# Performance work log

Measured on AMD Instinct MI355X. Metric: run time of the kernel, lower is better.

## Reference

```python
import jax, jax.numpy as jnp
import numpy as np

B, S, D = 32, 512, 512
H, DK, DV, DFF = 8, 64, 64, 2048
TEMP = float(np.sqrt(DK))  # d_k ** 0.5
COS_EPS = 1e-8             # torch.cosine_similarity eps
LN_EPS = 1e-5


def _layernorm(x, g, b):
    mu = jnp.mean(x, axis=-1, keepdims=True)
    var = jnp.var(x, axis=-1, keepdims=True)
    return (x - mu) * jax.lax.rsqrt(var + LN_EPS) * g + b


def setup_inputs() -> dict:
    key = jax.random.key(0)
    ks = jax.random.split(key, 12)
    s = 0.02
    return {
        "x": jax.random.normal(ks[0], (B, S, D), dtype=jnp.float32),
        "w_q": jax.random.normal(ks[1], (D, H * DK), dtype=jnp.float32) * s,
        "w_k": jax.random.normal(ks[2], (D, H * DK), dtype=jnp.float32) * s,
        "w_v": jax.random.normal(ks[3], (D, H * DV), dtype=jnp.float32) * s,
        "w_o": jax.random.normal(ks[4], (H * DV, D), dtype=jnp.float32) * s,
        "w_ff1": jax.random.normal(ks[5], (D, DFF), dtype=jnp.float32) * s,
        "b_ff1": jnp.zeros((DFF,), dtype=jnp.float32),
        "w_ff2": jax.random.normal(ks[6], (DFF, D), dtype=jnp.float32) * s,
        "b_ff2": jnp.zeros((D,), dtype=jnp.float32),
        "g1": jnp.ones((D,), dtype=jnp.float32),
        "b1": jnp.zeros((D,), dtype=jnp.float32),
        "g2": jnp.ones((D,), dtype=jnp.float32),
        "b2": jnp.zeros((D,), dtype=jnp.float32),
    }


def reference(x, w_q, w_k, w_v, w_o, w_ff1, b_ff1, w_ff2, b_ff2, g1, b1, g2, b2):
    b, s, _ = x.shape
    # projections -> [b, h, s, d]
    q = (x @ w_q).reshape(b, s, H, DK).transpose(0, 2, 1, 3)
    k = (x @ w_k).reshape(b, s, H, DK).transpose(0, 2, 1, 3)
    v = (x @ w_v).reshape(b, s, H, DV).transpose(0, 2, 1, 3)
    # cosine-similarity attention: dot(q,k) / max(||q||*||k||, eps) / temperature
    scores = jnp.einsum("bhqd,bhkd->bhqk", q, k)
    nq = jnp.linalg.norm(q, axis=-1)  # [b,h,s]
    nk = jnp.linalg.norm(k, axis=-1)
    denom = jnp.maximum(nq[:, :, :, None] * nk[:, :, None, :], COS_EPS)
    attn = jax.nn.softmax(scores / denom / TEMP, axis=-1)
    out = jnp.einsum("bhqk,bhkd->bhqd", attn, v)  # [b,h,s,dv]
    out = out.transpose(0, 2, 1, 3).reshape(b, s, H * DV) @ w_o
    # residual + LN1
    h1 = _layernorm(x + out, g1, b1)
    # FFN
    ffn = jax.nn.relu(h1 @ w_ff1 + b_ff1) @ w_ff2 + b_ff2
    # residual + LN2
    return _layernorm(h1 + ffn, g2, b2)
```

## Files before the change

kernel.cpp:

```cpp
#include <hip/hip_runtime.h>
#include <cmath>

typedef __bf16 bf16x8 __attribute__((ext_vector_type(8)));
typedef __bf16 bf16x4 __attribute__((ext_vector_type(4)));
typedef float  floatx4 __attribute__((ext_vector_type(4)));

#define LN_EPS 1e-5f
#define INV_TEMP 0.125f

static const int Mrows = 16384;

__device__ __forceinline__ void gload_lds16(const void* g, void* l) {
  __builtin_amdgcn_global_load_lds(
      (const __attribute__((address_space(1))) void*)g,
      (__attribute__((address_space(3))) void*)l, 16, 0, 0);
}

__global__ __launch_bounds__(256) void prep_kernel(const float* __restrict__ x, __bf16* __restrict__ xb,
                                                   const float* __restrict__ wq, const float* __restrict__ wk,
                                                   const float* __restrict__ wv, const float* __restrict__ wo,
                                                   const float* __restrict__ wff1, const float* __restrict__ wff2,
                                                   __bf16* __restrict__ tq, __bf16* __restrict__ tk,
                                                   __bf16* __restrict__ tv, __bf16* __restrict__ to_,
                                                   __bf16* __restrict__ tff1, __bf16* __restrict__ tff2) {
  const int bid = blockIdx.x, tid = threadIdx.x;
  if (bid < 8192) {
    int i = bid * 256 + tid;
    float4 v = ((const float4*)x)[i];
    __bf16* d = xb + i * 4;
    d[0] = (__bf16)v.x; d[1] = (__bf16)v.y; d[2] = (__bf16)v.z; d[3] = (__bf16)v.w;
    return;
  }
  __shared__ __bf16 til[64][72];
  int t = bid - 8192;
  const float* src; __bf16* dst; int R, C, bx, by;
  if (t < 256) {
    int w = t >> 6, tt = t & 63;
    const float* srcs[4] = {wq, wk, wv, wo};
    __bf16* dsts[4] = {tq, tk, tv, to_};
    src = srcs[w]; dst = dsts[w]; R = 512; C = 512; bx = tt & 7; by = tt >> 3;
  } else if (t < 512) {
    int tt = t - 256;
    src = wff1; dst = tff1; R = 512; C = 2048; bx = tt & 31; by = tt >> 5;
  } else {
    int tt = t - 512;
    src = wff2; dst = tff2; R = 2048; C = 512; bx = tt & 7; by = tt >> 3;
  }
  const float* s = src + (size_t)(by * 64) * C + bx * 64;
  int r = tid >> 4, c4 = (tid & 15) * 4;
  for (int p = 0; p < 4; ++p) {
    int rr = r + p * 16;
    float4 v = *(const float4*)(s + (size_t)rr * C + c4);
    til[c4 + 0][rr] = (__bf16)v.x;
    til[c4 + 1][rr] = (__bf16)v.y;
    til[c4 + 2][rr] = (__bf16)v.z;
    til[c4 + 3][rr] = (__bf16)v.w;
  }
  __syncthreads();
  __bf16* d = dst + (size_t)(bx * 64) * R + by * 64;
  int orow = tid >> 3, oc8 = (tid & 7) * 8;
  for (int p = 0; p < 2; ++p) {
    int rr = orow + p * 32;
    *(bf16x8*)(d + (size_t)rr * R + oc8) = *(const bf16x8*)(&til[rr][oc8]);
  }
}

template <int EPI, int NBN, int NDIM, int KDIM, int NKS>
__global__ __launch_bounds__(512, 2) void gemm256(const __bf16* __restrict__ A,
                                                  const __bf16* __restrict__ Bt,
                                                  __bf16* __restrict__ Cv,
                                                  const float* __restrict__ bias,
                                                  float* __restrict__ norms,
                                                  __bf16* __restrict__ vtg) {
  __shared__ __align__(16) char smem[131072];
  const int tid = threadIdx.x;
  const int wave = tid >> 6, lane = tid & 63;
  const int l15 = lane & 15, quad = lane >> 4;
  const int wm = wave >> 2, wn = wave & 3;

  constexpr int NBM = Mrows / 256;
  constexpr int NBLK = NBM * NBN * NKS;
  constexpr int KS = KDIM / NKS;
  constexpr int NTH = KS / 32;

  int id = blockIdx.x;
  int t = (id & 7) * (NBLK >> 3) + (id >> 3);
  const int ks = t / (NBM * NBN);
  t -= ks * (NBM * NBN);
  const int nblk = t % NBN, mblk = t / NBN;
  const int m0 = mblk * 256, n0 = nblk * 256;
  const __bf16* Ab = A + (size_t)ks * KS;
  const __bf16* Bb = Bt + (size_t)ks * KS;
  __bf16* Cw = Cv + (size_t)ks * Mrows * NDIM;
  (void)bias;

  const int wq = wave & 3, isB = wave >> 2;
  const int l3 = lane >> 3, s_ = lane & 7;
  const int rowst = wq * 64 + l3 * 2 + (s_ >> 2);
  const int ksw = (s_ & 3) ^ (l3 & 3);
  const __bf16* sbase = (isB ? Bb + (size_t)(n0 + rowst) * KDIM
                             : Ab + (size_t)(m0 + rowst) * KDIM) + ksw * 8;
  const int ldob = isB * 16384 + wq * 4096 + lane * 16;

  const int lrt = (l15 >> 1) * 128 + (((l15 & 1) * 4 + (quad ^ ((l15 >> 1) & 3))) * 16);
  const int aoff = wm * 8192;
  const int boff = 16384 + wn * 4096;

  floatx4 zero = {0.f, 0.f, 0.f, 0.f};
  floatx4 acc[8][4];
#pragma unroll
  for (int i = 0; i < 8; ++i)
#pragma unroll
    for (int j = 0; j < 4; ++j) acc[i][j] = zero;

#define STAGEH(h)                                                            \
  {                                                                          \
    _Pragma("unroll") for (int j = 0; j < 4; ++j)                            \
        gload_lds16(sbase + (size_t)j * (16 * KDIM) + (h) * 32,              \
                    smem + ((h) & 3) * 32768 + ldob + j * 1024);             \
  }

#define PHASE(h, VM, DOSTAGE)                                                \
  {                                                                          \
    asm volatile("s_waitcnt vmcnt(" #VM ")" ::: "memory");                   \
    __builtin_amdgcn_s_barrier();                                            \
    const char* slotp = smem + ((h) & 3) * 32768;                            \
    bf16x8 aF[8], bF[4];                                                     \
    _Pragma("unroll") for (int i = 0; i < 8; ++i)                            \
      aF[i] = *(const bf16x8*)(slotp + aoff + i * 1024 + lrt);               \
    _Pragma("unroll") for (int j = 0; j < 4; ++j)                            \
      bF[j] = *(const bf16x8*)(slotp + boff + j * 1024 + lrt);               \
    if (DOSTAGE) STAGEH((h) + 3);                                            \
    asm volatile("s_waitcnt lgkmcnt(0)" ::: "memory");                       \
    __builtin_amdgcn_s_setprio(1);                                           \
    _Pragma("unroll") for (int i = 0; i < 8; ++i)                            \
      _Pragma("unroll") for (int j = 0; j < 4; ++j)                          \
        acc[i][j] = __builtin_amdgcn_mfma_f32_16x16x32_bf16(aF[i], bF[j],    \
                                                            acc[i][j], 0, 0, 0); \
    __builtin_amdgcn_s_setprio(0);                                           \
  }

  STAGEH(0); STAGEH(1); STAGEH(2);

  for (int h = 0; h <= NTH - 4; ++h) PHASE(h, 8, 1);
  PHASE(NTH - 3, 8, 0);
  PHASE(NTH - 2, 4, 0);
  PHASE(NTH - 1, 0, 0);

#undef STAGEH
#undef PHASE

  if (EPI == 4) {
    int head_global = (n0 + wn * 64) >> 6;
    int kind = head_global >> 3;
    if (kind < 2) {
      int h = head_global & 7;
#pragma unroll
      for (int ii = 0; ii < 8; ++ii)
#pragma unroll
        for (int r = 0; r < 4; ++r) {
          float sq = 0.f;
#pragma unroll
          for (int jj = 0; jj < 4; ++jj) {
            float v = acc[ii][jj][r];
            sq += v * v;
          }
          for (int m = 1; m < 16; m <<= 1) sq += __shfl_xor(sq, m, 64);
          if (l15 == 0) {
            int arow = m0 + wm * 128 + ii * 16 + quad * 4 + r;
            int bb = arow >> 9, ss = arow & 511;
            norms[kind * 131072 + ((bb << 3) + h) * 512 + ss] = rsqrtf(sq);
          }
        }
    } else {
      const int PADT = 136;
      __bf16* Ct = (__bf16*)smem;
      int bb = m0 >> 9, s0r = m0 & 511;
#pragma unroll
      for (int hh = 0; hh < 2; ++hh) {
        __builtin_amdgcn_s_barrier();
        if (wm == hh) {
#pragma unroll
          for (int ii = 0; ii < 8; ++ii)
#pragma unroll
            for (int jj = 0; jj < 4; ++jj) {
              bf16x4 pk;
#pragma unroll
              for (int r = 0; r < 4; ++r) pk[r] = (__bf16)acc[ii][jj][r];
              *(bf16x4*)(Ct + (wn * 64 + jj * 16 + l15) * PADT + ii * 16 + quad * 4) = pk;
            }
        }
        __builtin_amdgcn_s_barrier();
#pragma unroll
        for (int p = 0; p < 8; ++p) {
          int c = p * 32 + (tid >> 4);
          int s8 = (tid & 15) * 8;
          int h = ((n0 + c) >> 6) & 7, d = c & 63;
          *(bf16x8*)(vtg + ((size_t)(((bb << 3) + h) * 64 + d)) * 512 + s0r + hh * 128 + s8) =
              *(const bf16x8*)(Ct + c * PADT + s8);
        }
      }
      return;
    }
  }

  const int PADC = 264;
  __bf16* Cs = (__bf16*)smem;
  float bv[4];
  if (EPI == 2) {
#pragma unroll
    for (int j = 0; j < 4; ++j) bv[j] = bias[n0 + wn * 64 + j * 16 + l15];
  }
#pragma unroll
  for (int hh = 0; hh < 2; ++hh) {
    __builtin_amdgcn_s_barrier();
    if (wm == hh) {
#pragma unroll
      for (int i = 0; i < 8; ++i)
#pragma unroll
        for (int j = 0; j < 4; ++j)
#pragma unroll
          for (int r = 0; r < 4; ++r) {
            float v = acc[i][j][r];
            if (EPI == 2) {
              v += bv[j];
              v = v > 0.f ? v : 0.f;
            }
            Cs[(i * 16 + quad * 4 + r) * PADC + wn * 64 + j * 16 + l15] = (__bf16)v;
          }
    }
    __builtin_amdgcn_s_barrier();
#pragma unroll
    for (int p = 0; p < 8; ++p) {
      int rowl = p * 16 + (tid >> 5);
      int c8 = (tid & 31) * 8;
      *(bf16x8*)(Cw + (size_t)(m0 + hh * 128 + rowl) * NDIM + n0 + c8) =
          *(const bf16x8*)(Cs + rowl * PADC + c8);
    }
  }
}

__global__ __launch_bounds__(256) void attn_kernel(const __bf16* __restrict__ qkv,
                                                   const __bf16* __restrict__ vtg,
                                                   const float* __restrict__ norms,
                                                   __bf16* __restrict__ out) {
  __shared__ __align__(16) __bf16 Ks[64 * 64];
  __shared__ __align__(16) __bf16 Vs[64 * 64];
  __shared__ __align__(16) __bf16 P2[4][16 * 72];
  const int tid = threadIdx.x, wave = tid >> 6, lane = tid & 63;
  const int l15 = lane & 15, quad = lane >> 4;
  const int bh = blockIdx.x & 255;
  const int qq = blockIdx.x >> 8;
  const int b = bh >> 3, h = bh & 7;
  const int qbase = qq * 128 + wave * 32;
  const int rs = lane >> 3;
  const int swz_st = ((lane & 7) ^ rs) * 8;
  const int s7 = l15 & 7;

  const __bf16* Qb = qkv + (size_t)(b * 512) * 1536 + h * 64;
  const __bf16* Kb = Qb + 512;
  const __bf16* Vtb = vtg + (size_t)bh * 32768;
  const float* nkinv = norms + 131072 + bh * 512;
  const float* nqinv = norms + bh * 512;
  __bf16* Pw = P2[wave];

  bf16x8 aq[2][2];
  float cq[2];
  for (int ch = 0; ch < 2; ++ch) {
    int qrow = qbase + ch * 16;
    aq[ch][0] = *(const bf16x8*)(Qb + (size_t)(qrow + l15) * 1536 + quad * 8);
    aq[ch][1] = *(const bf16x8*)(Qb + (size_t)(qrow + l15) * 1536 + 32 + quad * 8);
    cq[ch] = nqinv[qrow + l15] * INV_TEMP;
  }

  floatx4 zero = {0.f, 0.f, 0.f, 0.f};
  floatx4 o[2][4];
  float lsum[2] = {0.f, 0.f};
  for (int ch = 0; ch < 2; ++ch)
    for (int jd = 0; jd < 4; ++jd) o[ch][jd] = zero;

  for (int kt = 0; kt < 8; ++kt) {
    int s0 = kt * 64;
    __syncthreads();
    for (int c = 0; c < 4; ++c) {
      int g = wave * 4 + c;
      const __bf16* src;
      __bf16* dst;
      if (g < 8) {
        int sk = g * 8 + rs;
        src = Kb + (size_t)(s0 + sk) * 1536 + swz_st;
        dst = Ks + g * 512;
      } else {
        int g2 = g - 8;
        int d = g2 * 8 + rs;
        src = Vtb + (size_t)d * 512 + s0 + swz_st;
        dst = Vs + g2 * 512;
      }
      gload_lds16(src, dst + lane * 8);
    }
    __syncthreads();

    for (int ch = 0; ch < 2; ++ch) {
      floatx4 z[4];
      for (int j = 0; j < 4; ++j) {
        int r64 = (j * 16 + l15) * 64;
        bf16x8 k0 = *(const bf16x8*)(Ks + r64 + ((quad ^ s7) * 8));
        bf16x8 k1 = *(const bf16x8*)(Ks + r64 + (((4 + quad) ^ s7) * 8));
        floatx4 zz = zero;
        zz = __builtin_amdgcn_mfma_f32_16x16x32_bf16(k0, aq[ch][0], zz, 0, 0, 0);
        zz = __builtin_amdgcn_mfma_f32_16x16x32_bf16(k1, aq[ch][1], zz, 0, 0, 0);
        z[j] = zz;
      }
      for (int j = 0; j < 4; ++j) {
        floatx4 nk4 = *(const floatx4*)(nkinv + s0 + j * 16 + quad * 4);
        bf16x4 pk;
        for (int r = 0; r < 4; ++r) {
          float p = __expf(z[j][r] * cq[ch] * nk4[r]);
          lsum[ch] += p;
          pk[r] = (__bf16)p;
        }
        *(bf16x4*)(Pw + l15 * 72 + j * 16 + quad * 4) = pk;
      }
      bf16x8 ap0 = *(const bf16x8*)(Pw + l15 * 72 + quad * 8);
      bf16x8 ap1 = *(const bf16x8*)(Pw + l15 * 72 + 32 + quad * 8);
      for (int jd = 0; jd < 4; ++jd) {
        int r64 = (jd * 16 + l15) * 64;
        bf16x8 v0 = *(const bf16x8*)(Vs + r64 + ((quad ^ s7) * 8));
        bf16x8 v1 = *(const bf16x8*)(Vs + r64 + (((4 + quad) ^ s7) * 8));
        o[ch][jd] = __builtin_amdgcn_mfma_f32_16x16x32_bf16(v0, ap0, o[ch][jd], 0, 0, 0);
        o[ch][jd] = __builtin_amdgcn_mfma_f32_16x16x32_bf16(v1, ap1, o[ch][jd], 0, 0, 0);
      }
    }
  }

  for (int ch = 0; ch < 2; ++ch) {
    float s = lsum[ch];
    s += __shfl_xor(s, 16, 64);
    s += __shfl_xor(s, 32, 64);
    float inv = __builtin_amdgcn_rcpf(s);
    int q = qbase + ch * 16 + l15;
    __bf16* op = out + (size_t)(b * 512 + q) * 512 + h * 64;
    for (int jd = 0; jd < 4; ++jd) {
      bf16x4 pk;
      for (int r = 0; r < 4; ++r) pk[r] = (__bf16)(o[ch][jd][r] * inv);
      *(bf16x4*)(op + jd * 16 + quad * 4) = pk;
    }
  }
}

template <bool X1BF, bool WF, bool WB, bool DUAL>
__global__ __launch_bounds__(256) void resid_ln(const float* __restrict__ X1f,
                                                const __bf16* __restrict__ X1b,
                                                const __bf16* __restrict__ X2,
                                                const __bf16* __restrict__ X2b,
                                                const float* __restrict__ bias,
                                                const float* __restrict__ g,
                                                const float* __restrict__ be,
                                                float* __restrict__ outf,
                                                __bf16* __restrict__ outb) {
  int row = blockIdx.x * 4 + (threadIdx.x >> 6);
  int lane = threadIdx.x & 63;
  float v[8];
  bf16x8 b8 = *(const bf16x8*)(X2 + (size_t)row * 512 + lane * 8);
  if (X1BF) {
    bf16x8 a = *(const bf16x8*)(X1b + (size_t)row * 512 + lane * 8);
    for (int i = 0; i < 8; ++i) v[i] = (float)a[i] + (float)b8[i];
  } else {
    const float4* r1 = (const float4*)(X1f + (size_t)row * 512);
    float4 a0 = r1[lane * 2], a1 = r1[lane * 2 + 1];
    v[0] = a0.x; v[1] = a0.y; v[2] = a0.z; v[3] = a0.w;
    v[4] = a1.x; v[5] = a1.y; v[6] = a1.z; v[7] = a1.w;
    for (int i = 0; i < 8; ++i) v[i] += (float)b8[i];
  }
  if (DUAL) {
    bf16x8 c8 = *(const bf16x8*)(X2b + (size_t)row * 512 + lane * 8);
    for (int i = 0; i < 8; ++i) v[i] += (float)c8[i];
  }
  if (bias) {
    const float* bp = bias + lane * 8;
    for (int i = 0; i < 8; ++i) v[i] += bp[i];
  }
  float s = 0.f, sq = 0.f;
  for (int i = 0; i < 8; ++i) {
    s += v[i];
    sq += v[i] * v[i];
  }
  for (int m = 1; m < 64; m <<= 1) {
    s += __shfl_xor(s, m, 64);
    sq += __shfl_xor(sq, m, 64);
  }
  float mean = s * (1.f / 512.f);
  float var = sq * (1.f / 512.f) - mean * mean;
  float rstd = rsqrtf(var + LN_EPS);
  const float* gp = g + lane * 8;
  const float* bp2 = be + lane * 8;
  float o[8];
  for (int i = 0; i < 8; ++i) o[i] = (v[i] - mean) * rstd * gp[i] + bp2[i];
  if (WF) {
    float4 w0 = {o[0], o[1], o[2], o[3]}, w1 = {o[4], o[5], o[6], o[7]};
    ((float4*)(outf + (size_t)row * 512))[lane * 2] = w0;
    ((float4*)(outf + (size_t)row * 512))[lane * 2 + 1] = w1;
  }
  if (WB) {
    __bf16 tmp[8];
    for (int i = 0; i < 8; ++i) tmp[i] = (__bf16)o[i];
    *(bf16x8*)(outb + (size_t)row * 512 + lane * 8) = *(bf16x8*)tmp;
  }
}

extern "C" void kernel_launch(void* const* d_in, const int* in_sizes, int n_in,
                              void* d_out, int out_size, void* d_ws, size_t ws_size,
                              hipStream_t stream) {
  const float* x     = (const float*)d_in[0];
  const float* w_q   = (const float*)d_in[1];
  const float* w_k   = (const float*)d_in[2];
  const float* w_v   = (const float*)d_in[3];
  const float* w_o   = (const float*)d_in[4];
  const float* w_ff1 = (const float*)d_in[5];
  const float* b_ff1 = (const float*)d_in[6];
  const float* w_ff2 = (const float*)d_in[7];
  const float* b_ff2 = (const float*)d_in[8];
  const float* g1    = (const float*)d_in[9];
  const float* b1    = (const float*)d_in[10];
  const float* g2    = (const float*)d_in[11];
  const float* b2    = (const float*)d_in[12];
  float* out = (float*)d_out;

  char* ws = (char*)d_ws;
  size_t off = 0;
  auto alloc = [&](size_t bytes) -> void* {
    void* p = ws + off;
    off += (bytes + 255) & ~(size_t)255;
    return p;
  };
  __bf16* xb     = (__bf16*)alloc((size_t)Mrows * 512 * 2);
  __bf16* wt_qkv = (__bf16*)alloc((size_t)1536 * 512 * 2);
  __bf16* wt_o   = (__bf16*)alloc((size_t)512 * 512 * 2);
  __bf16* wt_ff1 = (__bf16*)alloc((size_t)2048 * 512 * 2);
  __bf16* wt_ff2 = (__bf16*)alloc((size_t)512 * 2048 * 2);
  __bf16* qkv    = (__bf16*)alloc((size_t)Mrows * 1536 * 2);
  float*  norms  = (float*)alloc((size_t)262144 * 4);
  __bf16* attn   = (__bf16*)alloc((size_t)Mrows * 512 * 2);
  __bf16* projb  = (__bf16*)alloc((size_t)Mrows * 512 * 2);
  __bf16* h1b    = (__bf16*)alloc((size_t)Mrows * 512 * 2);
  __bf16* mid    = (__bf16*)alloc((size_t)Mrows * 2048 * 2);
  __bf16* vtg    = mid;
  __bf16* wo_p   = mid;
  __bf16* f2o    = attn;

  prep_kernel<<<8960, 256, 0, stream>>>(x, xb, w_q, w_k, w_v, w_o, w_ff1, w_ff2,
                                        wt_qkv, wt_qkv + 512 * 512, wt_qkv + 2 * 512 * 512,
                                        wt_o, wt_ff1, wt_ff2);

  gemm256<4, 6, 1536, 512, 1><<<dim3(384), 512, 0, stream>>>(xb, wt_qkv, qkv, nullptr,
                                                             norms, vtg);
  attn_kernel<<<dim3(1024), 256, 0, stream>>>(qkv, vtg, norms, attn);
  gemm256<0, 2, 512, 512, 2><<<dim3(256), 512, 0, stream>>>(attn, wt_o, wo_p, nullptr,
                                                            nullptr, nullptr);
  resid_ln<false, false, true, true><<<4096, 256, 0, stream>>>(x, nullptr, wo_p,
                                                               wo_p + (size_t)Mrows * 512,
                                                               nullptr, g1, b1, nullptr, h1b);
  gemm256<2, 8, 2048, 512, 1><<<dim3(512), 512, 0, stream>>>(h1b, wt_ff1, mid, b_ff1,
                                                             nullptr, nullptr);
  gemm256<0, 2, 512, 2048, 2><<<dim3(256), 512, 0, stream>>>(mid, wt_ff2, f2o, nullptr,
                                                             nullptr, nullptr);
  resid_ln<true, true, false, true><<<4096, 256, 0, stream>>>(nullptr, h1b, f2o,
                                                              f2o + (size_t)Mrows * 512,
                                                              b_ff2, g2, b2, out, nullptr);
}
```

Baseline: 329.5 us.

## Shrink GEMM tile to 128x256 with double-buffered LDS for higher occupancy

The shared GEMM kernel moves from 256x256 block tiles with a four-slot LDS ring to 128x256 tiles with a two-slot double buffer. Each wave now stages three 16-row chunks, and the launch bound asks for four blocks per CU, so grids double and more blocks can be resident. Epilogues (norms, V transpose, bias/relu store) are resized to match. In exchange, the deeper prefetch pipeline becomes a full vmcnt(0) wait each phase, and there is less B-operand reuse per block.

Measured after the change: 321.2 us. -2.5%, faster.

```diff
diff --git a/kernel.cpp b/kernel.cpp
--- a/kernel.cpp
+++ b/kernel.cpp
@@ -66,19 +66,19 @@
 }
 
 template <int EPI, int NBN, int NDIM, int KDIM, int NKS>
-__global__ __launch_bounds__(512, 2) void gemm256(const __bf16* __restrict__ A,
+__global__ __launch_bounds__(512, 4) void gemm256(const __bf16* __restrict__ A,
                                                   const __bf16* __restrict__ Bt,
                                                   __bf16* __restrict__ Cv,
                                                   const float* __restrict__ bias,
                                                   float* __restrict__ norms,
                                                   __bf16* __restrict__ vtg) {
-  __shared__ __align__(16) char smem[131072];
+  __shared__ __align__(16) char smem[49152];
   const int tid = threadIdx.x;
   const int wave = tid >> 6, lane = tid & 63;
   const int l15 = lane & 15, quad = lane >> 4;
   const int wm = wave >> 2, wn = wave & 3;
 
-  constexpr int NBM = Mrows / 256;
+  constexpr int NBM = Mrows / 128;
   constexpr int NBLK = NBM * NBN * NKS;
   constexpr int KS = KDIM / NKS;
   constexpr int NTH = KS / 32;
@@ -88,64 +88,66 @@
   const int ks = t / (NBM * NBN);
   t -= ks * (NBM * NBN);
   const int nblk = t % NBN, mblk = t / NBN;
-  const int m0 = mblk * 256, n0 = nblk * 256;
+  const int m0 = mblk * 128, n0 = nblk * 256;
   const __bf16* Ab = A + (size_t)ks * KS;
   const __bf16* Bb = Bt + (size_t)ks * KS;
   __bf16* Cw = Cv + (size_t)ks * Mrows * NDIM;
   (void)bias;
 
-  const int wq = wave & 3, isB = wave >> 2;
   const int l3 = lane >> 3, s_ = lane & 7;
-  const int rowst = wq * 64 + l3 * 2 + (s_ >> 2);
+  const int rl = l3 * 2 + (s_ >> 2);
   const int ksw = (s_ & 3) ^ (l3 & 3);
-  const __bf16* sbase = (isB ? Bb + (size_t)(n0 + rowst) * KDIM
-                             : Ab + (size_t)(m0 + rowst) * KDIM) + ksw * 8;
-  const int ldob = isB * 16384 + wq * 4096 + lane * 16;
+  const __bf16* sb[3];
+  int ldo[3];
+#pragma unroll
+  for (int j = 0; j < 3; ++j) {
+    int c = wave * 3 + j;
+    int isB = c >= 8 ? 1 : 0;
+    int cc = c - isB * 8;
+    int row = cc * 16 + rl;
+    sb[j] = (isB ? Bb + (size_t)(n0 + row) * KDIM
+                 : Ab + (size_t)(m0 + row) * KDIM) + ksw * 8;
+    ldo[j] = isB * 8192 + cc * 1024 + lane * 16;
+  }
 
   const int lrt = (l15 >> 1) * 128 + (((l15 & 1) * 4 + (quad ^ ((l15 >> 1) & 3))) * 16);
-  const int aoff = wm * 8192;
-  const int boff = 16384 + wn * 4096;
 
   floatx4 zero = {0.f, 0.f, 0.f, 0.f};
-  floatx4 acc[8][4];
-#pragma unroll
-  for (int i = 0; i < 8; ++i)
+  floatx4 acc[4][4];
+#pragma unroll
+  for (int i = 0; i < 4; ++i)
 #pragma unroll
     for (int j = 0; j < 4; ++j) acc[i][j] = zero;
 
 #define STAGEH(h)                                                            \
   {                                                                          \
+    _Pragma("unroll") for (int j = 0; j < 3; ++j)                            \
+        gload_lds16(sb[j] + (h) * 32, smem + ((h) & 1) * 24576 + ldo[j]);    \
+  }
+
+#define PHASE(h, DOSTAGE)                                                    \
+  {                                                                          \
+    asm volatile("s_waitcnt vmcnt(0)" ::: "memory");                         \
+    __builtin_amdgcn_s_barrier();                                            \
+    const char* slotp = smem + ((h) & 1) * 24576;                            \
+    bf16x8 aF[4], bF[4];                                                     \
+    _Pragma("unroll") for (int i = 0; i < 4; ++i)                            \
+      aF[i] = *(const bf16x8*)(slotp + (wm * 4 + i) * 1024 + lrt);           \
     _Pragma("unroll") for (int j = 0; j < 4; ++j)                            \
-        gload_lds16(sbase + (size_t)j * (16 * KDIM) + (h) * 32,              \
-                    smem + ((h) & 3) * 32768 + ldob + j * 1024);             \
-  }
-
-#define PHASE(h, VM, DOSTAGE)                                                \
-  {                                                                          \
-    asm volatile("s_waitcnt vmcnt(" #VM ")" ::: "memory");                   \
-    __builtin_amdgcn_s_barrier();                                            \
-    const char* slotp = smem + ((h) & 3) * 32768;                            \
-    bf16x8 aF[8], bF[4];                                                     \
-    _Pragma("unroll") for (int i = 0; i < 8; ++i)                            \
-      aF[i] = *(const bf16x8*)(slotp + aoff + i * 1024 + lrt);               \
-    _Pragma("unroll") for (int j = 0; j < 4; ++j)                            \
-      bF[j] = *(const bf16x8*)(slotp + boff + j * 1024 + lrt);               \
-    if (DOSTAGE) STAGEH((h) + 3);                                            \
+      bF[j] = *(const bf16x8*)(slotp + 8192 + (wn * 4 + j) * 1024 + lrt);    \
+    if (DOSTAGE) STAGEH((h) + 1);                                            \
     asm volatile("s_waitcnt lgkmcnt(0)" ::: "memory");                       \
     __builtin_amdgcn_s_setprio(1);                                           \
-    _Pragma("unroll") for (int i = 0; i < 8; ++i)                            \
+    _Pragma("unroll") for (int i = 0; i < 4; ++i)                            \
       _Pragma("unroll") for (int j = 0; j < 4; ++j)                          \
         acc[i][j] = __builtin_amdgcn_mfma_f32_16x16x32_bf16(aF[i], bF[j],    \
                                                             acc[i][j], 0, 0, 0); \
     __builtin_amdgcn_s_setprio(0);                                           \
   }
 
-  STAGEH(0); STAGEH(1); STAGEH(2);
-
-  for (int h = 0; h <= NTH - 4; ++h) PHASE(h, 8, 1);
-  PHASE(NTH - 3, 8, 0);
-  PHASE(NTH - 2, 4, 0);
-  PHASE(NTH - 1, 0, 0);
+  STAGEH(0);
+  for (int h = 0; h < NTH - 1; ++h) PHASE(h, 1);
+  PHASE(NTH - 1, 0);
 
 #undef STAGEH
 #undef PHASE
@@ -156,7 +158,7 @@
     if (kind < 2) {
       int h = head_global & 7;
 #pragma unroll
-      for (int ii = 0; ii < 8; ++ii)
+      for (int ii = 0; ii < 4; ++ii)
 #pragma unroll
         for (int r = 0; r < 4; ++r) {
           float sq = 0.f;
@@ -167,13 +169,13 @@
           }
           for (int m = 1; m < 16; m <<= 1) sq += __shfl_xor(sq, m, 64);
           if (l15 == 0) {
-            int arow = m0 + wm * 128 + ii * 16 + quad * 4 + r;
+            int arow = m0 + wm * 64 + ii * 16 + quad * 4 + r;
             int bb = arow >> 9, ss = arow & 511;
             norms[kind * 131072 + ((bb << 3) + h) * 512 + ss] = rsqrtf(sq);
           }
         }
     } else {
-      const int PADT = 136;
+      const int PADT = 72;
       __bf16* Ct = (__bf16*)smem;
       int bb = m0 >> 9, s0r = m0 & 511;
 #pragma unroll
@@ -181,7 +183,7 @@
         __builtin_amdgcn_s_barrier();
         if (wm == hh) {
 #pragma unroll
-          for (int ii = 0; ii < 8; ++ii)
+          for (int ii = 0; ii < 4; ++ii)
 #pragma unroll
             for (int jj = 0; jj < 4; ++jj) {
               bf16x4 pk;
@@ -192,11 +194,11 @@
         }
         __builtin_amdgcn_s_barrier();
 #pragma unroll
-        for (int p = 0; p < 8; ++p) {
-          int c = p * 32 + (tid >> 4);
-          int s8 = (tid & 15) * 8;
+        for (int p = 0; p < 4; ++p) {
+          int c = p * 64 + (tid >> 3);
+          int s8 = (tid & 7) * 8;
           int h = ((n0 + c) >> 6) & 7, d = c & 63;
-          *(bf16x8*)(vtg + ((size_t)(((bb << 3) + h) * 64 + d)) * 512 + s0r + hh * 128 + s8) =
+          *(bf16x8*)(vtg + ((size_t)(((bb << 3) + h) * 64 + d)) * 512 + s0r + hh * 64 + s8) =
               *(const bf16x8*)(Ct + c * PADT + s8);
         }
       }
@@ -216,7 +218,7 @@
     __builtin_amdgcn_s_barrier();
     if (wm == hh) {
 #pragma unroll
-      for (int i = 0; i < 8; ++i)
+      for (int i = 0; i < 4; ++i)
 #pragma unroll
         for (int j = 0; j < 4; ++j)
 #pragma unroll
@@ -231,10 +233,10 @@
     }
     __builtin_amdgcn_s_barrier();
 #pragma unroll
-    for (int p = 0; p < 8; ++p) {
+    for (int p = 0; p < 4; ++p) {
       int rowl = p * 16 + (tid >> 5);
       int c8 = (tid & 31) * 8;
-      *(bf16x8*)(Cw + (size_t)(m0 + hh * 128 + rowl) * NDIM + n0 + c8) =
+      *(bf16x8*)(Cw + (size_t)(m0 + hh * 64 + rowl) * NDIM + n0 + c8) =
           *(const bf16x8*)(Cs + rowl * PADC + c8);
     }
   }
@@ -452,17 +454,17 @@
                                         wt_qkv, wt_qkv + 512 * 512, wt_qkv + 2 * 512 * 512,
                                         wt_o, wt_ff1, wt_ff2);
 
-  gemm256<4, 6, 1536, 512, 1><<<dim3(384), 512, 0, stream>>>(xb, wt_qkv, qkv, nullptr,
+  gemm256<4, 6, 1536, 512, 1><<<dim3(768), 512, 0, stream>>>(xb, wt_qkv, qkv, nullptr,
                                                              norms, vtg);
   attn_kernel<<<dim3(1024), 256, 0, stream>>>(qkv, vtg, norms, attn);
-  gemm256<0, 2, 512, 512, 2><<<dim3(256), 512, 0, stream>>>(attn, wt_o, wo_p, nullptr,
+  gemm256<0, 2, 512, 512, 2><<<dim3(512), 512, 0, stream>>>(attn, wt_o, wo_p, nullptr,
                                                             nullptr, nullptr);
   resid_ln<false, false, true, true><<<4096, 256, 0, stream>>>(x, nullptr, wo_p,
                                                                wo_p + (size_t)Mrows * 512,
                                                                nullptr, g1, b1, nullptr, h1b);
-  gemm256<2, 8, 2048, 512, 1><<<dim3(512), 512, 0, stream>>>(h1b, wt_ff1, mid, b_ff1,
-                                                             nullptr, nullptr);
-  gemm256<0, 2, 512, 2048, 2><<<dim3(256), 512, 0, stream>>>(mid, wt_ff2, f2o, nullptr,
+  gemm256<2, 8, 2048, 512, 1><<<dim3(1024), 512, 0, stream>>>(h1b, wt_ff1, mid, b_ff1,
+                                                              nullptr, nullptr);
+  gemm256<0, 2, 512, 2048, 2><<<dim3(512), 512, 0, stream>>>(mid, wt_ff2, f2o, nullptr,
                                                              nullptr, nullptr);
   resid_ln<true, true, false, true><<<4096, 256, 0, stream>>>(nullptr, h1b, f2o,
                                                               f2o + (size_t)Mrows * 512,
```
